# Performance work log

Measured on AMD Instinct MI355X. Metric: run time of the kernel, lower is better.

## Reference

```python
import jax, jax.numpy as jnp
import numpy as np

B, S, DM, H = 2, 2048, 1024, 16
HD = DM // H
SCALE = 1.0 / np.sqrt(HD)  # temperature = 1.0
LN_EPS = 1e-5


def setup_inputs() -> dict:
    key = jax.random.key(0)
    ks = jax.random.split(key, 12)
    s = 1.0 / np.sqrt(DM)
    inp = {
        'x': jax.random.normal(ks[0], (B, S, DM), dtype=jnp.float32),
        'Wq': jax.random.uniform(ks[1], (DM, DM), jnp.float32, -s, s),
        'bq': jnp.zeros((DM,), jnp.float32),
        'Wk': jax.random.uniform(ks[2], (DM, DM), jnp.float32, -s, s),
        'bk': jnp.zeros((DM,), jnp.float32),
        'Wv': jax.random.uniform(ks[3], (DM, DM), jnp.float32, -s, s),
        'bv': jnp.zeros((DM,), jnp.float32),
        'Wo': jax.random.uniform(ks[4], (DM, DM), jnp.float32, -s, s),
        'bo': jnp.zeros((DM,), jnp.float32),
        'Wg': jax.random.uniform(ks[5], (DM, DM), jnp.float32, -s, s),
        'bg': jnp.zeros((DM,), jnp.float32),
        'attention_weights': jnp.ones((H,), jnp.float32),
        'ln_gamma': jnp.ones((DM,), jnp.float32),
        'ln_beta': jnp.zeros((DM,), jnp.float32),
    }
    return inp


def _forward(x, Wq, bq, Wk, bk, Wv, bv, Wo, bo, Wg, bg, attention_weights, ln_gamma, ln_beta):
    # projections -> [B, H, S, HD]
    def split_heads(t):
        return t.reshape(B, S, H, HD).transpose(0, 2, 1, 3)
    q = split_heads(x @ Wq.T + bq)
    k = split_heads(x @ Wk.T + bk)
    v = split_heads(x @ Wv.T + bv)
    # scores [B, H, S, S]; no softmax: exact-erf GELU activation instead
    scores = jnp.einsum('bhsd,bhtd->bhst', q, k) * SCALE
    attn = jax.nn.gelu(scores, approximate=False)
    head_w = jax.nn.softmax(attention_weights)  # [H]
    attn = attn * head_w[None, :, None, None]
    # context [B, S, DM]
    ctx = jnp.einsum('bhst,bhtd->bhsd', attn, v).transpose(0, 2, 1, 3).reshape(B, S, DM)
    out = ctx @ Wo.T + bo
    gate = jax.nn.sigmoid(out @ Wg.T + bg)
    out = gate * out + (1.0 - gate) * x
    y = out + x
    mu = jnp.mean(y, axis=-1, keepdims=True)
    var = jnp.var(y, axis=-1, keepdims=True)
    return (y - mu) / jnp.sqrt(var + LN_EPS) * ln_gamma + ln_beta


def reference(x, Wq, bq, Wk, bk, Wv, bv, Wo, bo, Wg, bg, attention_weights, ln_gamma, ln_beta):
    return _forward(x, Wq, bq, Wk, bk, Wv, bv, Wo, bo, Wg, bg, attention_weights, ln_gamma, ln_beta)
```

## Files before the change

### kernel.cpp

```cpp
#include <hip/hip_runtime.h>
#include <hip/hip_bf16.h>

#define B_ 2
#define S_ 2048
#define DM_ 1024
#define H_ 16
#define HD_ 64
#define QKVLD 3072
#define WELT_ ((size_t)DM_ * DM_)

using bf16x8 = __attribute__((ext_vector_type(8))) short;
using f32x4  = __attribute__((ext_vector_type(4))) float;
using f32x16 = __attribute__((ext_vector_type(16))) float;

#define GLOAD16(g, l) __builtin_amdgcn_global_load_lds( \
    (const __attribute__((address_space(1))) void*)(g), \
    (__attribute__((address_space(3))) void*)(l), 16, 0, 0)

__device__ __forceinline__ int swz128(int row, int bytecol) {
    return row * 128 + (bytecol ^ ((row & 7) << 4));
}

__device__ __forceinline__ float gelu_poly(float x) {
    float u = x * x;
    float t = fmaf(-0.00074855f, u, 0.0146724f);
    t = fmaf(t, u, -0.1266945f);
    t = fmaf(t, u, 0.7966101f);
    float e = x * t;
    e = fminf(fmaxf(e, -1.0f), 1.0f);
    float hx = 0.5f * x;
    return fmaf(hx, e, hx);
}

__device__ __forceinline__ ushort bf16_rne(float f) {
    uint b = __builtin_bit_cast(uint, f);
    b += 0x7FFF + ((b >> 16) & 1);
    return (ushort)(b >> 16);
}

__device__ __forceinline__ float bf16_to_f(ushort u) {
    return __builtin_bit_cast(float, (uint)u << 16);
}

__device__ __forceinline__ uint cvtpk(float lo, float hi) {
    uint r;
    asm("v_cvt_pk_bf16_f32 %0, %1, %2" : "=v"(r) : "v"(lo), "v"(hi));
    return r;
}
__device__ __forceinline__ void pl32swap(uint& a, uint& b) {
    asm volatile("v_permlane32_swap_b32 %0, %1" : "+v"(a), "+v"(b));
}

__global__ __launch_bounds__(256) void cast_bf16_kernel(const float* __restrict__ in,
                                                        __hip_bfloat16* __restrict__ out, int n) {
    int i = (blockIdx.x * 256 + threadIdx.x) * 4;
    if (i >= n) return;
    float4 v = *(const float4*)(in + i);
    ushort4 o = { bf16_rne(v.x), bf16_rne(v.y), bf16_rne(v.z), bf16_rne(v.w) };
    *(ushort4*)(out + i) = o;
}

__global__ __launch_bounds__(256) void prep_kernel(
    const float* __restrict__ Wq, const float* __restrict__ Wk, const float* __restrict__ Wv,
    const float* __restrict__ Wo, const float* __restrict__ Wg,
    const float* __restrict__ bq, const float* __restrict__ bk, const float* __restrict__ bv,
    const float* __restrict__ aw, __hip_bfloat16* __restrict__ Wdst, float* __restrict__ bqkv)
{
    auto headw = [&](int h) {
        float mx = aw[0];
        for (int i = 1; i < H_; ++i) mx = fmaxf(mx, aw[i]);
        float sm = 0.f;
        for (int i = 0; i < H_; ++i) sm += expf(aw[i] - mx);
        return expf(aw[h] - mx) / sm;
    };
    int blk = blockIdx.x;
    if (blk < 5120) {
        int widx = blk >> 10;
        int row = blk & 1023;
        int off = row * 1024 + threadIdx.x * 4;
        const float* src = widx == 0 ? Wq : widx == 1 ? Wk : widx == 2 ? Wv : widx == 3 ? Wo : Wg;
        float scale = widx == 0 ? 0.125f : 1.0f;
        if (widx == 2) scale = headw(row >> 6);
        float4 v = *(const float4*)(src + off);
        ushort4 o = { bf16_rne(v.x * scale), bf16_rne(v.y * scale),
                      bf16_rne(v.z * scale), bf16_rne(v.w * scale) };
        *(ushort4*)(Wdst + widx * WELT_ + off) = o;
    } else {
        int i = (blk - 5120) * 256 + threadIdx.x;
        if (i < 3 * DM_) {
            float v;
            if (i < DM_) v = bq[i] * 0.125f;
            else if (i < 2 * DM_) v = bk[i - DM_];
            else v = bv[i - 2 * DM_] * headw((i - 2 * DM_) >> 6);
            bqkv[i] = v;
        }
    }
}

__global__ __launch_bounds__(256, 2) void gemm_nt_kernel(
    const __hip_bfloat16* __restrict__ A, int lda,
    const __hip_bfloat16* __restrict__ Bw, int ldb,
    const float* __restrict__ bias, float* __restrict__ Cf,
    __hip_bfloat16* __restrict__ Cb, int ldc, int M, int N, int K)
{
    __shared__ __align__(16) char smem[32768];
    const int tid = threadIdx.x;
    const int w = tid >> 6, lane = tid & 63, hi = lane >> 4, lo = lane & 15;
    const int wr = w >> 1, wc = w & 1;
    const int m0 = blockIdx.y * 128, n0 = blockIdx.x * 128;

    const int srow = lane >> 3;
    const int scol = (lane & 7) ^ srow;
    const __hip_bfloat16* sbase;
    int sld;
    char* lbase;
    if (w < 2) {
        sbase = A + (size_t)(m0 + w * 64 + srow) * lda + scol * 8;
        sld = lda;
        lbase = smem + w * 8192;
    } else {
        sbase = Bw + (size_t)(n0 + (w - 2) * 64 + srow) * ldb + scol * 8;
        sld = ldb;
        lbase = smem + 16384 + (w - 2) * 8192;
    }

    f32x4 acc[4][4];
#pragma unroll
    for (int m = 0; m < 4; ++m)
#pragma unroll
        for (int n = 0; n < 4; ++n) acc[m][n] = (f32x4){0.f, 0.f, 0.f, 0.f};

    for (int k0 = 0; k0 < K; k0 += 64) {
#pragma unroll
        for (int i = 0; i < 8; ++i)
            GLOAD16(sbase + (size_t)i * 8 * sld + k0, lbase + i * 1024);
        __syncthreads();
#pragma unroll
        for (int ks = 0; ks < 2; ++ks) {
            bf16x8 af[4], bfr[4];
#pragma unroll
            for (int m = 0; m < 4; ++m)
                af[m] = *(const bf16x8*)(smem + swz128(wr * 64 + m * 16 + lo, ks * 64 + hi * 16));
#pragma unroll
            for (int n = 0; n < 4; ++n)
                bfr[n] = *(const bf16x8*)(smem + 16384 + swz128(wc * 64 + n * 16 + lo, ks * 64 + hi * 16));
#pragma unroll
            for (int m = 0; m < 4; ++m)
#pragma unroll
                for (int n = 0; n < 4; ++n)
                    acc[m][n] = __builtin_amdgcn_mfma_f32_16x16x32_bf16(af[m], bfr[n], acc[m][n], 0, 0, 0);
        }
        __syncthreads();
    }

#pragma unroll
    for (int n = 0; n < 4; ++n) {
        int gc = n0 + wc * 64 + n * 16 + lo;
        float bz = bias[gc];
#pragma unroll
        for (int m = 0; m < 4; ++m) {
            int gr = m0 + wr * 64 + m * 16 + hi * 4;
#pragma unroll
            for (int r = 0; r < 4; ++r) {
                float v = acc[m][n][r] + bz;
                size_t o = (size_t)(gr + r) * ldc + gc;
                if (Cf) Cf[o] = v;
                if (Cb) *(ushort*)(Cb + o) = bf16_rne(v);
            }
        }
    }
}

__global__ __launch_bounds__(256) void transpose_v_kernel(const __hip_bfloat16* __restrict__ QKV,
                                                          __hip_bfloat16* __restrict__ Vt) {
    __shared__ __align__(16) ushort tile[64][80];
    const int tid = threadIdx.x;
    const int nt = S_ / 64;
    const int blk = blockIdx.x;
    const int t0 = (blk % nt) * 64;
    const int bh = blk / nt;
    const int h = bh % H_, b = bh / H_;
#pragma unroll
    for (int c = tid; c < 512; c += 256) {
        int row = c >> 3, cg = c & 7;
        float4 v = *(const float4*)(QKV + (size_t)(b * S_ + t0 + row) * QKVLD + 2 * DM_ + h * HD_ + cg * 8);
        *(float4*)(&tile[row][cg * 8]) = v;
    }
    __syncthreads();
#pragma unroll
    for (int c = tid; c < 512; c += 256) {
        int d = c >> 3, tg = c & 7;
        union { ushort u[8]; float4 v; } tmp;
#pragma unroll
        for (int j = 0; j < 8; ++j) tmp.u[j] = tile[tg * 8 + j][d];
        *(float4*)(Vt + ((size_t)(b * H_ + h) * HD_ + d) * S_ + t0 + tg * 8) = tmp.v;
    }
}

__global__ __launch_bounds__(256) void attn_kernel(
    const __hip_bfloat16* __restrict__ QKV, const __hip_bfloat16* __restrict__ Vt,
    __hip_bfloat16* __restrict__ ctx)
{
    __shared__ __align__(16) char lds[2][16384];

    const int tid = threadIdx.x;
    const int w = tid >> 6, lane = tid & 63;
    const int l31 = lane & 31, hi2 = lane >> 5;
    const int nq = S_ / 128;
    int blk = blockIdx.x;
    blk = (blk & 7) * 64 + (blk >> 3);
    const int q0 = (blk % nq) * 128;
    const int bh = blk / nq;
    const int h = bh % H_, b = bh / H_;

    bf16x8 qf[4];
    {
        const __hip_bfloat16* qrow = QKV + ((size_t)(b * S_ + q0 + w * 32 + l31) * QKVLD + h * HD_);
#pragma unroll
        for (int ks = 0; ks < 4; ++ks)
            qf[ks] = *(const bf16x8*)(qrow + ks * 16 + hi2 * 8);
    }

    const bool isK = (w < 2);
    const int fb = (w & 1) * 4;
    const __hip_bfloat16* sp[4];
    int ldsoff[4];
#pragma unroll
    for (int j = 0; j < 4; ++j) {
        int f = fb + j;
        if (isK) {
            sp[j] = QKV + (size_t)(b * S_ + (f >> 2) * 32 + l31) * QKVLD + DM_ + h * HD_ + (f & 3) * 16 + hi2 * 8;
            ldsoff[j] = f * 1024;
        } else {
            sp[j] = Vt + ((size_t)((b * H_ + h) * HD_) + (f >> 2) * 32 + l31) * S_ + (f & 3) * 16 + hi2 * 8;
            ldsoff[j] = 8192 + f * 1024;
        }
    }
    const size_t tstep = isK ? (size_t)64 * QKVLD : (size_t)64;

#define STAGE(buf) do { \
    _Pragma("unroll") \
    for (int j = 0; j < 4; ++j) { \
        GLOAD16(sp[j], lds[buf] + ldsoff[j]); \
        sp[j] += tstep; \
    } } while (0)

    f32x16 cacc[2];
#pragma unroll
    for (int n = 0; n < 2; ++n)
#pragma unroll
        for (int r = 0; r < 16; ++r) cacc[n][r] = 0.f;

    STAGE(0);
    asm volatile("s_waitcnt vmcnt(0)" ::: "memory");
    __builtin_amdgcn_s_barrier();

    const int lane16 = lane * 16;
    for (int t = 0; t < S_ / 64; ++t) {
        const int cur = t & 1;
        if (t + 1 < S_ / 64) STAGE(cur ^ 1);

#pragma unroll
        for (int n = 0; n < 2; ++n) {
            f32x16 sacc;
#pragma unroll
            for (int r = 0; r < 16; ++r) sacc[r] = 0.f;
#pragma unroll
            for (int ks = 0; ks < 4; ++ks) {
                bf16x8 kf = *(const bf16x8*)(lds[cur] + (n * 4 + ks) * 1024 + lane16);
                sacc = __builtin_amdgcn_mfma_f32_32x32x16_bf16(kf, qf[ks], sacc, 0, 0, 0);
            }
            float p[16];
#pragma unroll
            for (int r = 0; r < 16; ++r) p[r] = gelu_poly(sacc[r]);
            uint a0 = cvtpk(p[0], p[1]),   b0 = cvtpk(p[4], p[5]);
            uint a1 = cvtpk(p[2], p[3]),   b1 = cvtpk(p[6], p[7]);
            uint a2 = cvtpk(p[8], p[9]),   b2 = cvtpk(p[12], p[13]);
            uint a3 = cvtpk(p[10], p[11]), b3 = cvtpk(p[14], p[15]);
            pl32swap(a0, b0); pl32swap(a1, b1); pl32swap(a2, b2); pl32swap(a3, b3);
            union { uint u[4]; bf16x8 v; } pa0, pa1;
            pa0.u[0] = a0; pa0.u[1] = a1; pa0.u[2] = b0; pa0.u[3] = b1;
            pa1.u[0] = a2; pa1.u[1] = a3; pa1.u[2] = b2; pa1.u[3] = b3;
#pragma unroll
            for (int kc2 = 0; kc2 < 2; ++kc2) {
                int kc = n * 2 + kc2;
                bf16x8 pa = kc2 ? pa1.v : pa0.v;
#pragma unroll
                for (int n2 = 0; n2 < 2; ++n2) {
                    bf16x8 vf = *(const bf16x8*)(lds[cur] + 8192 + (n2 * 4 + kc) * 1024 + lane16);
                    cacc[n2] = __builtin_amdgcn_mfma_f32_32x32x16_bf16(pa, vf, cacc[n2], 0, 0, 0);
                }
            }
        }
        asm volatile("s_waitcnt vmcnt(0)" ::: "memory");
        __builtin_amdgcn_s_barrier();
    }

#pragma unroll
    for (int n2 = 0; n2 < 2; ++n2)
#pragma unroll
        for (int r = 0; r < 16; ++r) {
            int qrow = (r & 3) + 8 * (r >> 2) + 4 * hi2;
            size_t o = (size_t)(b * S_ + q0 + w * 32 + qrow) * DM_ + h * HD_ + n2 * 32 + l31;
            *(ushort*)(ctx + o) = bf16_rne(cacc[n2][r]);
        }
#undef STAGE
}

__global__ __launch_bounds__(256) void epilogue_ln_kernel(
    const __hip_bfloat16* __restrict__ outb, const __hip_bfloat16* __restrict__ gpreb,
    const float* __restrict__ x, const float* __restrict__ gamma,
    const float* __restrict__ beta, float* __restrict__ y)
{
    const int row = blockIdx.x, tid = threadIdx.x;
    const size_t base = (size_t)row * DM_ + tid * 4;
    ushort4 ob = *(const ushort4*)(outb + base);
    ushort4 gb = *(const ushort4*)(gpreb + base);
    float4 xv = *(const float4*)(x + base);
    float yv[4];
    float s = 0.f, s2 = 0.f;
    const ushort* obp = (const ushort*)&ob;
    const ushort* gbp = (const ushort*)&gb;
#pragma unroll
    for (int j = 0; j < 4; ++j) {
        float o = bf16_to_f(obp[j]), g = bf16_to_f(gbp[j]), xx = ((float*)&xv)[j];
        float gate = __builtin_amdgcn_rcpf(1.f + __expf(-g));
        float yy = gate * o + (1.f - gate) * xx + xx;
        yv[j] = yy;
        s += yy; s2 += yy * yy;
    }
    const int w = tid >> 6, lane = tid & 63;
#pragma unroll
    for (int off = 32; off > 0; off >>= 1) {
        s  += __shfl_down(s, off, 64);
        s2 += __shfl_down(s2, off, 64);
    }
    __shared__ float red[8];
    if (lane == 0) { red[w] = s; red[4 + w] = s2; }
    __syncthreads();
    s  = red[0] + red[1] + red[2] + red[3];
    s2 = red[4] + red[5] + red[6] + red[7];
    const float mu = s * (1.f / DM_);
    const float var = s2 * (1.f / DM_) - mu * mu;
    const float rstd = rsqrtf(var + 1e-5f);
    float4 outv;
#pragma unroll
    for (int j = 0; j < 4; ++j) {
        int col = tid * 4 + j;
        ((float*)&outv)[j] = (yv[j] - mu) * rstd * gamma[col] + beta[col];
    }
    *(float4*)(y + base) = outv;
}

extern "C" void kernel_launch(void* const* d_in, const int* in_sizes, int n_in,
                              void* d_out, int out_size, void* d_ws, size_t ws_size,
                              hipStream_t stream) {
    const float* x  = (const float*)d_in[0];
    const float* Wq = (const float*)d_in[1];
    const float* bq = (const float*)d_in[2];
    const float* Wk = (const float*)d_in[3];
    const float* bk = (const float*)d_in[4];
    const float* Wv = (const float*)d_in[5];
    const float* bv = (const float*)d_in[6];
    const float* Wo = (const float*)d_in[7];
    const float* bo = (const float*)d_in[8];
    const float* Wg = (const float*)d_in[9];
    const float* bg = (const float*)d_in[10];
    const float* aw = (const float*)d_in[11];
    const float* gamma = (const float*)d_in[12];
    const float* beta  = (const float*)d_in[13];

    char* ws = (char*)d_ws;
    size_t off = 0;
    auto alloc = [&](size_t bytes) -> char* {
        char* p = ws + off;
        off += (bytes + 255) & ~(size_t)255;
        return p;
    };
    const size_t NTOK = (size_t)B_ * S_;
    const size_t NELT = NTOK * DM_;

    __hip_bfloat16* xb    = (__hip_bfloat16*)alloc(NELT * 2);
    __hip_bfloat16* Wall  = (__hip_bfloat16*)alloc(5 * WELT_ * 2);
    float*          bqkv  = (float*)alloc(3 * DM_ * 4);
    __hip_bfloat16* qkvb  = (__hip_bfloat16*)alloc(NTOK * QKVLD * 2);
    __hip_bfloat16* Vtb   = (__hip_bfloat16*)alloc(NELT * 2);
    __hip_bfloat16* ctxb  = (__hip_bfloat16*)alloc(NELT * 2);
    __hip_bfloat16* outb  = (__hip_bfloat16*)alloc(NELT * 2);
    __hip_bfloat16* gpreb = (__hip_bfloat16*)alloc(NELT * 2);

    cast_bf16_kernel<<<(int)(NELT / 1024), 256, 0, stream>>>(x, xb, (int)NELT);
    prep_kernel<<<5120 + 12, 256, 0, stream>>>(Wq, Wk, Wv, Wo, Wg, bq, bk, bv, aw, Wall, bqkv);

    gemm_nt_kernel<<<dim3(QKVLD / 128, (int)(NTOK / 128)), 256, 0, stream>>>(
        xb, DM_, Wall, DM_, bqkv, nullptr, qkvb, QKVLD, (int)NTOK, QKVLD, DM_);

    transpose_v_kernel<<<B_ * H_ * (S_ / 64), 256, 0, stream>>>(qkvb, Vtb);
    attn_kernel<<<B_ * H_ * (S_ / 128), 256, 0, stream>>>(qkvb, Vtb, ctxb);

    gemm_nt_kernel<<<dim3(DM_ / 128, (int)(NTOK / 128)), 256, 0, stream>>>(
        ctxb, DM_, Wall + 3 * WELT_, DM_, bo, nullptr, outb, DM_, (int)NTOK, DM_, DM_);
    gemm_nt_kernel<<<dim3(DM_ / 128, (int)(NTOK / 128)), 256, 0, stream>>>(
        outb, DM_, Wall + 4 * WELT_, DM_, bg, nullptr, gpreb, DM_, (int)NTOK, DM_, DM_);

    epilogue_ln_kernel<<<(int)NTOK, 256, 0, stream>>>(outb, gpreb, x, gamma, beta, (float*)d_out);
}
```

Before: 162.1 us.

## Fold Wo into gate weights, triple-buffer attention, pack GELU math

Precomputes a combined weight Wg·Wo (via a small 1024^3 GEMM on transposed Wo) and a combined bias, so the output and gate projections become one N=2048 GEMM on ctx instead of two dependent GEMMs. The x cast is merged into the prep kernel to save a launch. The attention loop moves from double to triple buffering with a partial vmcnt wait, and the GELU polynomial uses packed f32 mul/fma instructions. Folding the weights changes the rounding path (gate input now comes from a bf16 product matrix), and the extra LDS buffer may lower attention occupancy.

Result: slower. 172.2 us (+6.3%).

```diff
diff --git a/kernel.cpp b/kernel.cpp
--- a/kernel.cpp
+++ b/kernel.cpp
@@ -10,6 +10,7 @@
 #define WELT_ ((size_t)DM_ * DM_)
 
 using bf16x8 = __attribute__((ext_vector_type(8))) short;
+using f32x2  = __attribute__((ext_vector_type(2))) float;
 using f32x4  = __attribute__((ext_vector_type(4))) float;
 using f32x16 = __attribute__((ext_vector_type(16))) float;
 
@@ -19,17 +20,6 @@
 
 __device__ __forceinline__ int swz128(int row, int bytecol) {
     return row * 128 + (bytecol ^ ((row & 7) << 4));
-}
-
-__device__ __forceinline__ float gelu_poly(float x) {
-    float u = x * x;
-    float t = fmaf(-0.00074855f, u, 0.0146724f);
-    t = fmaf(t, u, -0.1266945f);
-    t = fmaf(t, u, 0.7966101f);
-    float e = x * t;
-    e = fminf(fmaxf(e, -1.0f), 1.0f);
-    float hx = 0.5f * x;
-    return fmaf(hx, e, hx);
 }
 
 __device__ __forceinline__ ushort bf16_rne(float f) {
@@ -50,21 +40,24 @@
 __device__ __forceinline__ void pl32swap(uint& a, uint& b) {
     asm volatile("v_permlane32_swap_b32 %0, %1" : "+v"(a), "+v"(b));
 }
-
-__global__ __launch_bounds__(256) void cast_bf16_kernel(const float* __restrict__ in,
-                                                        __hip_bfloat16* __restrict__ out, int n) {
-    int i = (blockIdx.x * 256 + threadIdx.x) * 4;
-    if (i >= n) return;
-    float4 v = *(const float4*)(in + i);
-    ushort4 o = { bf16_rne(v.x), bf16_rne(v.y), bf16_rne(v.z), bf16_rne(v.w) };
-    *(ushort4*)(out + i) = o;
+__device__ __forceinline__ f32x2 pk_mul(f32x2 a, f32x2 b) {
+    f32x2 d;
+    asm("v_pk_mul_f32 %0, %1, %2" : "=v"(d) : "v"(a), "v"(b));
+    return d;
+}
+__device__ __forceinline__ f32x2 pk_fma(f32x2 a, f32x2 b, f32x2 c) {
+    f32x2 d;
+    asm("v_pk_fma_f32 %0, %1, %2, %3" : "=v"(d) : "v"(a), "v"(b), "v"(c));
+    return d;
 }
 
 __global__ __launch_bounds__(256) void prep_kernel(
+    const float* __restrict__ x, __hip_bfloat16* __restrict__ xb,
     const float* __restrict__ Wq, const float* __restrict__ Wk, const float* __restrict__ Wv,
     const float* __restrict__ Wo, const float* __restrict__ Wg,
     const float* __restrict__ bq, const float* __restrict__ bk, const float* __restrict__ bv,
-    const float* __restrict__ aw, __hip_bfloat16* __restrict__ Wdst, float* __restrict__ bqkv)
+    const float* __restrict__ aw, __hip_bfloat16* __restrict__ Wall,
+    __hip_bfloat16* __restrict__ Wcomb, float* __restrict__ bqkv)
 {
     auto headw = [&](int h) {
         float mx = aw[0];
@@ -74,19 +67,27 @@
         return expf(aw[h] - mx) / sm;
     };
     int blk = blockIdx.x;
-    if (blk < 5120) {
+    if (blk < 4096) {
+        int i = blk * 1024 + threadIdx.x * 4;
+        float4 v = *(const float4*)(x + i);
+        ushort4 o = { bf16_rne(v.x), bf16_rne(v.y), bf16_rne(v.z), bf16_rne(v.w) };
+        *(ushort4*)(xb + i) = o;
+    } else if (blk < 9216) {
+        blk -= 4096;
         int widx = blk >> 10;
         int row = blk & 1023;
         int off = row * 1024 + threadIdx.x * 4;
         const float* src = widx == 0 ? Wq : widx == 1 ? Wk : widx == 2 ? Wv : widx == 3 ? Wo : Wg;
         float scale = widx == 0 ? 0.125f : 1.0f;
         if (widx == 2) scale = headw(row >> 6);
+        __hip_bfloat16* dst = (widx == 3) ? Wcomb
+                            : Wall + (size_t)(widx == 4 ? 3 : widx) * WELT_;
         float4 v = *(const float4*)(src + off);
         ushort4 o = { bf16_rne(v.x * scale), bf16_rne(v.y * scale),
                       bf16_rne(v.z * scale), bf16_rne(v.w * scale) };
-        *(ushort4*)(Wdst + widx * WELT_ + off) = o;
+        *(ushort4*)(dst + off) = o;
     } else {
-        int i = (blk - 5120) * 256 + threadIdx.x;
+        int i = (blk - 9216) * 256 + threadIdx.x;
         if (i < 3 * DM_) {
             float v;
             if (i < DM_) v = bq[i] * 0.125f;
@@ -95,6 +96,45 @@
             bqkv[i] = v;
         }
     }
+}
+
+__global__ __launch_bounds__(256) void transpose_wo_kernel(const float* __restrict__ Wo,
+                                                           __hip_bfloat16* __restrict__ Wot) {
+    __shared__ ushort tile[64][72];
+    const int tid = threadIdx.x;
+    const int c0 = blockIdx.x * 64, r0 = blockIdx.y * 64;
+#pragma unroll
+    for (int c = tid; c < 1024; c += 256) {
+        int row = c >> 4, cg = c & 15;
+        float4 v = *(const float4*)(Wo + (size_t)(r0 + row) * 1024 + c0 + cg * 4);
+        tile[row][cg * 4 + 0] = bf16_rne(v.x);
+        tile[row][cg * 4 + 1] = bf16_rne(v.y);
+        tile[row][cg * 4 + 2] = bf16_rne(v.z);
+        tile[row][cg * 4 + 3] = bf16_rne(v.w);
+    }
+    __syncthreads();
+#pragma unroll
+    for (int c = tid; c < 512; c += 256) {
+        int d = c >> 3, tg = c & 7;
+        union { ushort u[8]; float4 v; } tmp;
+#pragma unroll
+        for (int j = 0; j < 8; ++j) tmp.u[j] = tile[tg * 8 + j][d];
+        *(float4*)(Wot + (size_t)(c0 + d) * 1024 + r0 + tg * 8) = tmp.v;
+    }
+}
+
+__global__ __launch_bounds__(256) void bias2_kernel(const float* __restrict__ Wg,
+                                                    const float* __restrict__ bo,
+                                                    const float* __restrict__ bg,
+                                                    float* __restrict__ bcomb) {
+    const int tid = threadIdx.x, w = tid >> 6, lane = tid & 63;
+    if (blockIdx.x < 4) bcomb[blockIdx.x * 256 + tid] = bo[blockIdx.x * 256 + tid];
+    const int row = blockIdx.x * 4 + w;
+    float s = 0.f;
+    for (int k = lane; k < 1024; k += 64) s += Wg[row * 1024 + k] * bo[k];
+#pragma unroll
+    for (int off = 32; off > 0; off >>= 1) s += __shfl_down(s, off, 64);
+    if (lane == 0) bcomb[1024 + row] = bg[row] + s;
 }
 
 __global__ __launch_bounds__(256, 2) void gemm_nt_kernel(
@@ -156,7 +196,7 @@
 #pragma unroll
     for (int n = 0; n < 4; ++n) {
         int gc = n0 + wc * 64 + n * 16 + lo;
-        float bz = bias[gc];
+        float bz = bias ? bias[gc] : 0.f;
 #pragma unroll
         for (int m = 0; m < 4; ++m) {
             int gr = m0 + wr * 64 + m * 16 + hi * 4;
@@ -201,7 +241,7 @@
     const __hip_bfloat16* __restrict__ QKV, const __hip_bfloat16* __restrict__ Vt,
     __hip_bfloat16* __restrict__ ctx)
 {
-    __shared__ __align__(16) char lds[2][16384];
+    __shared__ __align__(16) char lds[3 * 16384];
 
     const int tid = threadIdx.x;
     const int w = tid >> 6, lane = tid & 63;
@@ -238,28 +278,28 @@
     }
     const size_t tstep = isK ? (size_t)64 * QKVLD : (size_t)64;
 
-#define STAGE(buf) do { \
+#define STAGE(base) do { \
     _Pragma("unroll") \
     for (int j = 0; j < 4; ++j) { \
-        GLOAD16(sp[j], lds[buf] + ldsoff[j]); \
+        GLOAD16(sp[j], (base) + ldsoff[j]); \
         sp[j] += tstep; \
     } } while (0)
 
+    const f32x2 PC3 = {-0.00074855f, -0.00074855f};
+    const f32x2 PC2 = { 0.0146724f,   0.0146724f};
+    const f32x2 PC1 = {-0.1266945f,  -0.1266945f};
+    const f32x2 PC0 = { 0.7966101f,   0.7966101f};
+    const f32x2 PHALF = {0.5f, 0.5f};
+
     f32x16 cacc[2];
 #pragma unroll
     for (int n = 0; n < 2; ++n)
 #pragma unroll
         for (int r = 0; r < 16; ++r) cacc[n][r] = 0.f;
 
-    STAGE(0);
-    asm volatile("s_waitcnt vmcnt(0)" ::: "memory");
-    __builtin_amdgcn_s_barrier();
-
     const int lane16 = lane * 16;
-    for (int t = 0; t < S_ / 64; ++t) {
-        const int cur = t & 1;
-        if (t + 1 < S_ / 64) STAGE(cur ^ 1);
-
+
+    auto compute_tile = [&](const char* cbase) {
 #pragma unroll
         for (int n = 0; n < 2; ++n) {
             f32x16 sacc;
@@ -267,16 +307,27 @@
             for (int r = 0; r < 16; ++r) sacc[r] = 0.f;
 #pragma unroll
             for (int ks = 0; ks < 4; ++ks) {
-                bf16x8 kf = *(const bf16x8*)(lds[cur] + (n * 4 + ks) * 1024 + lane16);
+                bf16x8 kf = *(const bf16x8*)(cbase + (n * 4 + ks) * 1024 + lane16);
                 sacc = __builtin_amdgcn_mfma_f32_32x32x16_bf16(kf, qf[ks], sacc, 0, 0, 0);
             }
-            float p[16];
-#pragma unroll
-            for (int r = 0; r < 16; ++r) p[r] = gelu_poly(sacc[r]);
-            uint a0 = cvtpk(p[0], p[1]),   b0 = cvtpk(p[4], p[5]);
-            uint a1 = cvtpk(p[2], p[3]),   b1 = cvtpk(p[6], p[7]);
-            uint a2 = cvtpk(p[8], p[9]),   b2 = cvtpk(p[12], p[13]);
-            uint a3 = cvtpk(p[10], p[11]), b3 = cvtpk(p[14], p[15]);
+            f32x2 P[8];
+#pragma unroll
+            for (int i = 0; i < 8; ++i) {
+                f32x2 xv = { sacc[2 * i], sacc[2 * i + 1] };
+                f32x2 u  = pk_mul(xv, xv);
+                f32x2 tt = pk_fma(PC3, u, PC2);
+                tt = pk_fma(tt, u, PC1);
+                tt = pk_fma(tt, u, PC0);
+                f32x2 e  = pk_mul(xv, tt);
+                e[0] = fminf(fmaxf(e[0], -1.f), 1.f);
+                e[1] = fminf(fmaxf(e[1], -1.f), 1.f);
+                f32x2 hx = pk_mul(xv, PHALF);
+                P[i] = pk_fma(hx, e, hx);
+            }
+            uint a0 = cvtpk(P[0][0], P[0][1]), b0 = cvtpk(P[2][0], P[2][1]);
+            uint a1 = cvtpk(P[1][0], P[1][1]), b1 = cvtpk(P[3][0], P[3][1]);
+            uint a2 = cvtpk(P[4][0], P[4][1]), b2 = cvtpk(P[6][0], P[6][1]);
+            uint a3 = cvtpk(P[5][0], P[5][1]), b3 = cvtpk(P[7][0], P[7][1]);
             pl32swap(a0, b0); pl32swap(a1, b1); pl32swap(a2, b2); pl32swap(a3, b3);
             union { uint u[4]; bf16x8 v; } pa0, pa1;
             pa0.u[0] = a0; pa0.u[1] = a1; pa0.u[2] = b0; pa0.u[3] = b1;
@@ -287,14 +338,31 @@
                 bf16x8 pa = kc2 ? pa1.v : pa0.v;
 #pragma unroll
                 for (int n2 = 0; n2 < 2; ++n2) {
-                    bf16x8 vf = *(const bf16x8*)(lds[cur] + 8192 + (n2 * 4 + kc) * 1024 + lane16);
+                    bf16x8 vf = *(const bf16x8*)(cbase + 8192 + (n2 * 4 + kc) * 1024 + lane16);
                     cacc[n2] = __builtin_amdgcn_mfma_f32_32x32x16_bf16(pa, vf, cacc[n2], 0, 0, 0);
                 }
             }
         }
-        asm volatile("s_waitcnt vmcnt(0)" ::: "memory");
+    };
+
+    const int NT = S_ / 64;
+    STAGE(lds);
+    STAGE(lds + 16384);
+
+    int cur = 0;
+    for (int t = 0; t < NT - 1; ++t) {
+        asm volatile("s_waitcnt vmcnt(4)" ::: "memory");
         __builtin_amdgcn_s_barrier();
-    }
+        if (t + 2 < NT) {
+            int nb = cur + 2; if (nb >= 3) nb -= 3;
+            STAGE(lds + nb * 16384);
+        }
+        compute_tile(lds + cur * 16384);
+        cur = (cur == 2) ? 0 : cur + 1;
+    }
+    asm volatile("s_waitcnt vmcnt(0)" ::: "memory");
+    __builtin_amdgcn_s_barrier();
+    compute_tile(lds + cur * 16384);
 
 #pragma unroll
     for (int n2 = 0; n2 < 2; ++n2)
@@ -308,15 +376,16 @@
 }
 
 __global__ __launch_bounds__(256) void epilogue_ln_kernel(
-    const __hip_bfloat16* __restrict__ outb, const __hip_bfloat16* __restrict__ gpreb,
-    const float* __restrict__ x, const float* __restrict__ gamma,
-    const float* __restrict__ beta, float* __restrict__ y)
+    const __hip_bfloat16* __restrict__ og, const float* __restrict__ x,
+    const float* __restrict__ gamma, const float* __restrict__ beta,
+    float* __restrict__ y)
 {
     const int row = blockIdx.x, tid = threadIdx.x;
-    const size_t base = (size_t)row * DM_ + tid * 4;
-    ushort4 ob = *(const ushort4*)(outb + base);
-    ushort4 gb = *(const ushort4*)(gpreb + base);
-    float4 xv = *(const float4*)(x + base);
+    const size_t obase = (size_t)row * 2048 + tid * 4;
+    const size_t xbase = (size_t)row * DM_ + tid * 4;
+    ushort4 ob = *(const ushort4*)(og + obase);
+    ushort4 gb = *(const ushort4*)(og + obase + 1024);
+    float4 xv = *(const float4*)(x + xbase);
     float yv[4];
     float s = 0.f, s2 = 0.f;
     const ushort* obp = (const ushort*)&ob;
@@ -349,7 +418,7 @@
         int col = tid * 4 + j;
         ((float*)&outv)[j] = (yv[j] - mu) * rstd * gamma[col] + beta[col];
     }
-    *(float4*)(y + base) = outv;
+    *(float4*)(y + xbase) = outv;
 }
 
 extern "C" void kernel_launch(void* const* d_in, const int* in_sizes, int n_in,
@@ -381,16 +450,24 @@
     const size_t NELT = NTOK * DM_;
 
     __hip_bfloat16* xb    = (__hip_bfloat16*)alloc(NELT * 2);
-    __hip_bfloat16* Wall  = (__hip_bfloat16*)alloc(5 * WELT_ * 2);
+    __hip_bfloat16* Wall  = (__hip_bfloat16*)alloc(4 * WELT_ * 2);
+    __hip_bfloat16* Wot   = (__hip_bfloat16*)alloc(WELT_ * 2);
+    __hip_bfloat16* Wcomb = (__hip_bfloat16*)alloc(2 * WELT_ * 2);
     float*          bqkv  = (float*)alloc(3 * DM_ * 4);
+    float*          bcomb = (float*)alloc(2 * DM_ * 4);
     __hip_bfloat16* qkvb  = (__hip_bfloat16*)alloc(NTOK * QKVLD * 2);
     __hip_bfloat16* Vtb   = (__hip_bfloat16*)alloc(NELT * 2);
     __hip_bfloat16* ctxb  = (__hip_bfloat16*)alloc(NELT * 2);
-    __hip_bfloat16* outb  = (__hip_bfloat16*)alloc(NELT * 2);
-    __hip_bfloat16* gpreb = (__hip_bfloat16*)alloc(NELT * 2);
-
-    cast_bf16_kernel<<<(int)(NELT / 1024), 256, 0, stream>>>(x, xb, (int)NELT);
-    prep_kernel<<<5120 + 12, 256, 0, stream>>>(Wq, Wk, Wv, Wo, Wg, bq, bk, bv, aw, Wall, bqkv);
+    __hip_bfloat16* ogb   = (__hip_bfloat16*)alloc(NTOK * 2048 * 2);
+
+    prep_kernel<<<9216 + 12, 256, 0, stream>>>(x, xb, Wq, Wk, Wv, Wo, Wg,
+                                               bq, bk, bv, aw, Wall, Wcomb, bqkv);
+    transpose_wo_kernel<<<dim3(16, 16), 256, 0, stream>>>(Wo, Wot);
+    bias2_kernel<<<256, 256, 0, stream>>>(Wg, bo, bg, bcomb);
+
+    gemm_nt_kernel<<<dim3(8, 8), 256, 0, stream>>>(
+        Wall + 3 * WELT_, DM_, Wot, DM_, nullptr, nullptr,
+        Wcomb + WELT_, DM_, DM_, DM_, DM_);
 
     gemm_nt_kernel<<<dim3(QKVLD / 128, (int)(NTOK / 128)), 256, 0, stream>>>(
         xb, DM_, Wall, DM_, bqkv, nullptr, qkvb, QKVLD, (int)NTOK, QKVLD, DM_);
@@ -398,10 +475,8 @@
     transpose_v_kernel<<<B_ * H_ * (S_ / 64), 256, 0, stream>>>(qkvb, Vtb);
     attn_kernel<<<B_ * H_ * (S_ / 128), 256, 0, stream>>>(qkvb, Vtb, ctxb);
 
-    gemm_nt_kernel<<<dim3(DM_ / 128, (int)(NTOK / 128)), 256, 0, stream>>>(
-        ctxb, DM_, Wall + 3 * WELT_, DM_, bo, nullptr, outb, DM_, (int)NTOK, DM_, DM_);
-    gemm_nt_kernel<<<dim3(DM_ / 128, (int)(NTOK / 128)), 256, 0, stream>>>(
-        outb, DM_, Wall + 4 * WELT_, DM_, bg, nullptr, gpreb, DM_, (int)NTOK, DM_, DM_);
-
-    epilogue_ln_kernel<<<(int)NTOK, 256, 0, stream>>>(outb, gpreb, x, gamma, beta, (float*)d_out);
-}
+    gemm_nt_kernel<<<dim3(2048 / 128, (int)(NTOK / 128)), 256, 0, stream>>>(
+        ctxb, DM_, Wcomb, DM_, bcomb, nullptr, ogb, 2048, (int)NTOK, 2048, DM_);
+
+    epilogue_ln_kernel<<<(int)NTOK, 256, 0, stream>>>(ogb, x, gamma, beta, (float*)d_out);
+}
```

## Fold gate projection into output GEMM and enlarge attention key tiles

Applied to the files above, without the earlier changes.

Precomputes Wg·Wo and bg+Wg·bo so that one N=2048 GEMM yields both the output and the gate pre-activation. This removes the dependent second 1024-wide GEMM and its intermediate buffer, at the cost of extra GEMM blocks that build the combined weight. The x cast is merged into the prep kernel, which also transposes Wo. The attention loop now stages 128-key tiles with double buffering and raises wave priority around the MFMA work. The epilogue reads the bf16 copy of x for the residual, which trades some accuracy for less memory traffic, and GELU clamping uses fmed3.

New measurement: 149.6 us. -7.7%, faster.

```diff
diff --git a/kernel.cpp b/kernel.cpp
--- a/kernel.cpp
+++ b/kernel.cpp
@@ -26,8 +26,7 @@
     float t = fmaf(-0.00074855f, u, 0.0146724f);
     t = fmaf(t, u, -0.1266945f);
     t = fmaf(t, u, 0.7966101f);
-    float e = x * t;
-    e = fminf(fmaxf(e, -1.0f), 1.0f);
+    float e = __builtin_amdgcn_fmed3f(x * t, -1.0f, 1.0f);
     float hx = 0.5f * x;
     return fmaf(hx, e, hx);
 }
@@ -51,21 +50,17 @@
     asm volatile("v_permlane32_swap_b32 %0, %1" : "+v"(a), "+v"(b));
 }
 
-__global__ __launch_bounds__(256) void cast_bf16_kernel(const float* __restrict__ in,
-                                                        __hip_bfloat16* __restrict__ out, int n) {
-    int i = (blockIdx.x * 256 + threadIdx.x) * 4;
-    if (i >= n) return;
-    float4 v = *(const float4*)(in + i);
-    ushort4 o = { bf16_rne(v.x), bf16_rne(v.y), bf16_rne(v.z), bf16_rne(v.w) };
-    *(ushort4*)(out + i) = o;
-}
-
 __global__ __launch_bounds__(256) void prep_kernel(
+    const float* __restrict__ x, __hip_bfloat16* __restrict__ xb,
     const float* __restrict__ Wq, const float* __restrict__ Wk, const float* __restrict__ Wv,
     const float* __restrict__ Wo, const float* __restrict__ Wg,
     const float* __restrict__ bq, const float* __restrict__ bk, const float* __restrict__ bv,
-    const float* __restrict__ aw, __hip_bfloat16* __restrict__ Wdst, float* __restrict__ bqkv)
+    const float* __restrict__ bo, const float* __restrict__ bg,
+    const float* __restrict__ aw, __hip_bfloat16* __restrict__ Wall,
+    __hip_bfloat16* __restrict__ Wcomb, __hip_bfloat16* __restrict__ Wot,
+    float* __restrict__ bqkv, float* __restrict__ bcomb)
 {
+    __shared__ ushort stile[64][72];
     auto headw = [&](int h) {
         float mx = aw[0];
         for (int i = 1; i < H_; ++i) mx = fmaxf(mx, aw[i]);
@@ -73,20 +68,29 @@
         for (int i = 0; i < H_; ++i) sm += expf(aw[i] - mx);
         return expf(aw[h] - mx) / sm;
     };
+    const int tid = threadIdx.x;
     int blk = blockIdx.x;
-    if (blk < 5120) {
+    if (blk < 4096) {
+        int i = blk * 1024 + tid * 4;
+        float4 v = *(const float4*)(x + i);
+        ushort4 o = { bf16_rne(v.x), bf16_rne(v.y), bf16_rne(v.z), bf16_rne(v.w) };
+        *(ushort4*)(xb + i) = o;
+    } else if (blk < 9216) {
+        blk -= 4096;
         int widx = blk >> 10;
         int row = blk & 1023;
-        int off = row * 1024 + threadIdx.x * 4;
+        int off = row * 1024 + tid * 4;
         const float* src = widx == 0 ? Wq : widx == 1 ? Wk : widx == 2 ? Wv : widx == 3 ? Wo : Wg;
         float scale = widx == 0 ? 0.125f : 1.0f;
         if (widx == 2) scale = headw(row >> 6);
+        __hip_bfloat16* dst = (widx == 3) ? Wcomb
+                            : Wall + (size_t)(widx == 4 ? 3 : widx) * WELT_;
         float4 v = *(const float4*)(src + off);
         ushort4 o = { bf16_rne(v.x * scale), bf16_rne(v.y * scale),
                       bf16_rne(v.z * scale), bf16_rne(v.w * scale) };
-        *(ushort4*)(Wdst + widx * WELT_ + off) = o;
-    } else {
-        int i = (blk - 5120) * 256 + threadIdx.x;
+        *(ushort4*)(dst + off) = o;
+    } else if (blk < 9228) {
+        int i = (blk - 9216) * 256 + tid;
         if (i < 3 * DM_) {
             float v;
             if (i < DM_) v = bq[i] * 0.125f;
@@ -94,6 +98,37 @@
             else v = bv[i - 2 * DM_] * headw((i - 2 * DM_) >> 6);
             bqkv[i] = v;
         }
+    } else if (blk < 9484) {
+        int idx = blk - 9228;
+        const int c0 = (idx & 15) * 64, r0 = (idx >> 4) * 64;
+#pragma unroll
+        for (int c = tid; c < 1024; c += 256) {
+            int row = c >> 4, cg = c & 15;
+            float4 v = *(const float4*)(Wo + (size_t)(r0 + row) * 1024 + c0 + cg * 4);
+            stile[row][cg * 4 + 0] = bf16_rne(v.x);
+            stile[row][cg * 4 + 1] = bf16_rne(v.y);
+            stile[row][cg * 4 + 2] = bf16_rne(v.z);
+            stile[row][cg * 4 + 3] = bf16_rne(v.w);
+        }
+        __syncthreads();
+#pragma unroll
+        for (int c = tid; c < 512; c += 256) {
+            int d = c >> 3, tg = c & 7;
+            union { ushort u[8]; float4 v; } tmp;
+#pragma unroll
+            for (int j = 0; j < 8; ++j) tmp.u[j] = stile[tg * 8 + j][d];
+            *(float4*)(Wot + (size_t)(c0 + d) * 1024 + r0 + tg * 8) = tmp.v;
+        }
+    } else {
+        int idx = blk - 9484;
+        const int w = tid >> 6, lane = tid & 63;
+        if (idx < 4) bcomb[idx * 256 + tid] = bo[idx * 256 + tid];
+        const int row = idx * 4 + w;
+        float s = 0.f;
+        for (int k = lane; k < 1024; k += 64) s += Wg[row * 1024 + k] * bo[k];
+#pragma unroll
+        for (int off = 32; off > 0; off >>= 1) s += __shfl_down(s, off, 64);
+        if (lane == 0) bcomb[1024 + row] = bg[row] + s;
     }
 }
 
@@ -101,13 +136,32 @@
     const __hip_bfloat16* __restrict__ A, int lda,
     const __hip_bfloat16* __restrict__ Bw, int ldb,
     const float* __restrict__ bias, float* __restrict__ Cf,
-    __hip_bfloat16* __restrict__ Cb, int ldc, int M, int N, int K)
+    __hip_bfloat16* __restrict__ Cb, int ldc, int K, int gx1, int nblk1,
+    const __hip_bfloat16* __restrict__ A2, const __hip_bfloat16* __restrict__ B2,
+    __hip_bfloat16* __restrict__ C2)
 {
     __shared__ __align__(16) char smem[32768];
     const int tid = threadIdx.x;
     const int w = tid >> 6, lane = tid & 63, hi = lane >> 4, lo = lane & 15;
     const int wr = w >> 1, wc = w & 1;
-    const int m0 = blockIdx.y * 128, n0 = blockIdx.x * 128;
+
+    const int bid = blockIdx.x;
+    const __hip_bfloat16 *Ap, *Bp;
+    const float* bp;
+    float* cf;
+    __hip_bfloat16* cb;
+    int LDA, LDB, LDC, KK, bx, by;
+    if (bid < nblk1) {
+        bx = bid % gx1; by = bid / gx1;
+        Ap = A; Bp = Bw; bp = bias; cf = Cf; cb = Cb;
+        LDA = lda; LDB = ldb; LDC = ldc; KK = K;
+    } else {
+        int t2 = bid - nblk1;
+        bx = t2 & 7; by = t2 >> 3;
+        Ap = A2; Bp = B2; bp = nullptr; cf = nullptr; cb = C2;
+        LDA = DM_; LDB = DM_; LDC = DM_; KK = DM_;
+    }
+    const int m0 = by * 128, n0 = bx * 128;
 
     const int srow = lane >> 3;
     const int scol = (lane & 7) ^ srow;
@@ -115,12 +169,12 @@
     int sld;
     char* lbase;
     if (w < 2) {
-        sbase = A + (size_t)(m0 + w * 64 + srow) * lda + scol * 8;
-        sld = lda;
+        sbase = Ap + (size_t)(m0 + w * 64 + srow) * LDA + scol * 8;
+        sld = LDA;
         lbase = smem + w * 8192;
     } else {
-        sbase = Bw + (size_t)(n0 + (w - 2) * 64 + srow) * ldb + scol * 8;
-        sld = ldb;
+        sbase = Bp + (size_t)(n0 + (w - 2) * 64 + srow) * LDB + scol * 8;
+        sld = LDB;
         lbase = smem + 16384 + (w - 2) * 8192;
     }
 
@@ -130,7 +184,7 @@
 #pragma unroll
         for (int n = 0; n < 4; ++n) acc[m][n] = (f32x4){0.f, 0.f, 0.f, 0.f};
 
-    for (int k0 = 0; k0 < K; k0 += 64) {
+    for (int k0 = 0; k0 < KK; k0 += 64) {
 #pragma unroll
         for (int i = 0; i < 8; ++i)
             GLOAD16(sbase + (size_t)i * 8 * sld + k0, lbase + i * 1024);
@@ -156,16 +210,16 @@
 #pragma unroll
     for (int n = 0; n < 4; ++n) {
         int gc = n0 + wc * 64 + n * 16 + lo;
-        float bz = bias[gc];
+        float bz = bp ? bp[gc] : 0.f;
 #pragma unroll
         for (int m = 0; m < 4; ++m) {
             int gr = m0 + wr * 64 + m * 16 + hi * 4;
 #pragma unroll
             for (int r = 0; r < 4; ++r) {
                 float v = acc[m][n][r] + bz;
-                size_t o = (size_t)(gr + r) * ldc + gc;
-                if (Cf) Cf[o] = v;
-                if (Cb) *(ushort*)(Cb + o) = bf16_rne(v);
+                size_t o = (size_t)(gr + r) * LDC + gc;
+                if (cf) cf[o] = v;
+                if (cb) *(ushort*)(cb + o) = bf16_rne(v);
             }
         }
     }
@@ -201,7 +255,7 @@
     const __hip_bfloat16* __restrict__ QKV, const __hip_bfloat16* __restrict__ Vt,
     __hip_bfloat16* __restrict__ ctx)
 {
-    __shared__ __align__(16) char lds[2][16384];
+    __shared__ __align__(16) char lds[2][32768];
 
     const int tid = threadIdx.x;
     const int w = tid >> 6, lane = tid & 63;
@@ -222,26 +276,26 @@
     }
 
     const bool isK = (w < 2);
-    const int fb = (w & 1) * 4;
-    const __hip_bfloat16* sp[4];
-    int ldsoff[4];
-#pragma unroll
-    for (int j = 0; j < 4; ++j) {
-        int f = fb + j;
+    const int f0 = (w & 1) * 8;
+    const __hip_bfloat16* sp[8];
+    int loff[8];
+#pragma unroll
+    for (int j = 0; j < 8; ++j) {
+        int f = f0 + j;
         if (isK) {
             sp[j] = QKV + (size_t)(b * S_ + (f >> 2) * 32 + l31) * QKVLD + DM_ + h * HD_ + (f & 3) * 16 + hi2 * 8;
-            ldsoff[j] = f * 1024;
+            loff[j] = f * 1024;
         } else {
-            sp[j] = Vt + ((size_t)((b * H_ + h) * HD_) + (f >> 2) * 32 + l31) * S_ + (f & 3) * 16 + hi2 * 8;
-            ldsoff[j] = 8192 + f * 1024;
-        }
-    }
-    const size_t tstep = isK ? (size_t)64 * QKVLD : (size_t)64;
+            sp[j] = Vt + ((size_t)((b * H_ + h) * HD_) + (f >> 3) * 32 + l31) * S_ + (f & 7) * 16 + hi2 * 8;
+            loff[j] = 16384 + f * 1024;
+        }
+    }
+    const size_t tstep = isK ? (size_t)128 * QKVLD : (size_t)128;
 
 #define STAGE(buf) do { \
     _Pragma("unroll") \
-    for (int j = 0; j < 4; ++j) { \
-        GLOAD16(sp[j], lds[buf] + ldsoff[j]); \
+    for (int j = 0; j < 8; ++j) { \
+        GLOAD16(sp[j], lds[buf] + loff[j]); \
         sp[j] += tstep; \
     } } while (0)
 
@@ -256,18 +310,20 @@
     __builtin_amdgcn_s_barrier();
 
     const int lane16 = lane * 16;
-    for (int t = 0; t < S_ / 64; ++t) {
+    const int NT = S_ / 128;
+    for (int t = 0; t < NT; ++t) {
         const int cur = t & 1;
-        if (t + 1 < S_ / 64) STAGE(cur ^ 1);
-
-#pragma unroll
-        for (int n = 0; n < 2; ++n) {
+        if (t + 1 < NT) STAGE(cur ^ 1);
+
+        __builtin_amdgcn_s_setprio(1);
+#pragma unroll
+        for (int tc = 0; tc < 4; ++tc) {
             f32x16 sacc;
 #pragma unroll
             for (int r = 0; r < 16; ++r) sacc[r] = 0.f;
 #pragma unroll
             for (int ks = 0; ks < 4; ++ks) {
-                bf16x8 kf = *(const bf16x8*)(lds[cur] + (n * 4 + ks) * 1024 + lane16);
+                bf16x8 kf = *(const bf16x8*)(lds[cur] + (tc * 4 + ks) * 1024 + lane16);
                 sacc = __builtin_amdgcn_mfma_f32_32x32x16_bf16(kf, qf[ks], sacc, 0, 0, 0);
             }
             float p[16];
@@ -283,15 +339,16 @@
             pa1.u[0] = a2; pa1.u[1] = a3; pa1.u[2] = b2; pa1.u[3] = b3;
 #pragma unroll
             for (int kc2 = 0; kc2 < 2; ++kc2) {
-                int kc = n * 2 + kc2;
+                int kc = tc * 2 + kc2;
                 bf16x8 pa = kc2 ? pa1.v : pa0.v;
 #pragma unroll
                 for (int n2 = 0; n2 < 2; ++n2) {
-                    bf16x8 vf = *(const bf16x8*)(lds[cur] + 8192 + (n2 * 4 + kc) * 1024 + lane16);
+                    bf16x8 vf = *(const bf16x8*)(lds[cur] + 16384 + (n2 * 8 + kc) * 1024 + lane16);
                     cacc[n2] = __builtin_amdgcn_mfma_f32_32x32x16_bf16(pa, vf, cacc[n2], 0, 0, 0);
                 }
             }
         }
+        __builtin_amdgcn_s_setprio(0);
         asm volatile("s_waitcnt vmcnt(0)" ::: "memory");
         __builtin_amdgcn_s_barrier();
     }
@@ -308,22 +365,24 @@
 }
 
 __global__ __launch_bounds__(256) void epilogue_ln_kernel(
-    const __hip_bfloat16* __restrict__ outb, const __hip_bfloat16* __restrict__ gpreb,
-    const float* __restrict__ x, const float* __restrict__ gamma,
-    const float* __restrict__ beta, float* __restrict__ y)
+    const __hip_bfloat16* __restrict__ og, const __hip_bfloat16* __restrict__ xb,
+    const float* __restrict__ gamma, const float* __restrict__ beta,
+    float* __restrict__ y)
 {
     const int row = blockIdx.x, tid = threadIdx.x;
-    const size_t base = (size_t)row * DM_ + tid * 4;
-    ushort4 ob = *(const ushort4*)(outb + base);
-    ushort4 gb = *(const ushort4*)(gpreb + base);
-    float4 xv = *(const float4*)(x + base);
+    const size_t obase = (size_t)row * 2048 + tid * 4;
+    const size_t xbase = (size_t)row * DM_ + tid * 4;
+    ushort4 ob = *(const ushort4*)(og + obase);
+    ushort4 gb = *(const ushort4*)(og + obase + 1024);
+    ushort4 xv = *(const ushort4*)(xb + xbase);
     float yv[4];
     float s = 0.f, s2 = 0.f;
     const ushort* obp = (const ushort*)&ob;
     const ushort* gbp = (const ushort*)&gb;
+    const ushort* xp  = (const ushort*)&xv;
 #pragma unroll
     for (int j = 0; j < 4; ++j) {
-        float o = bf16_to_f(obp[j]), g = bf16_to_f(gbp[j]), xx = ((float*)&xv)[j];
+        float o = bf16_to_f(obp[j]), g = bf16_to_f(gbp[j]), xx = bf16_to_f(xp[j]);
         float gate = __builtin_amdgcn_rcpf(1.f + __expf(-g));
         float yy = gate * o + (1.f - gate) * xx + xx;
         yv[j] = yy;
@@ -349,7 +408,7 @@
         int col = tid * 4 + j;
         ((float*)&outv)[j] = (yv[j] - mu) * rstd * gamma[col] + beta[col];
     }
-    *(float4*)(y + base) = outv;
+    *(float4*)(y + xbase) = outv;
 }
 
 extern "C" void kernel_launch(void* const* d_in, const int* in_sizes, int n_in,
@@ -381,27 +440,30 @@
     const size_t NELT = NTOK * DM_;
 
     __hip_bfloat16* xb    = (__hip_bfloat16*)alloc(NELT * 2);
-    __hip_bfloat16* Wall  = (__hip_bfloat16*)alloc(5 * WELT_ * 2);
+    __hip_bfloat16* Wall  = (__hip_bfloat16*)alloc(4 * WELT_ * 2);
+    __hip_bfloat16* Wot   = (__hip_bfloat16*)alloc(WELT_ * 2);
+    __hip_bfloat16* Wcomb = (__hip_bfloat16*)alloc(2 * WELT_ * 2);
     float*          bqkv  = (float*)alloc(3 * DM_ * 4);
+    float*          bcomb = (float*)alloc(2 * DM_ * 4);
     __hip_bfloat16* qkvb  = (__hip_bfloat16*)alloc(NTOK * QKVLD * 2);
     __hip_bfloat16* Vtb   = (__hip_bfloat16*)alloc(NELT * 2);
     __hip_bfloat16* ctxb  = (__hip_bfloat16*)alloc(NELT * 2);
-    __hip_bfloat16* outb  = (__hip_bfloat16*)alloc(NELT * 2);
-    __hip_bfloat16* gpreb = (__hip_bfloat16*)alloc(NELT * 2);
-
-    cast_bf16_kernel<<<(int)(NELT / 1024), 256, 0, stream>>>(x, xb, (int)NELT);
-    prep_kernel<<<5120 + 12, 256, 0, stream>>>(Wq, Wk, Wv, Wo, Wg, bq, bk, bv, aw, Wall, bqkv);
-
-    gemm_nt_kernel<<<dim3(QKVLD / 128, (int)(NTOK / 128)), 256, 0, stream>>>(
-        xb, DM_, Wall, DM_, bqkv, nullptr, qkvb, QKVLD, (int)NTOK, QKVLD, DM_);
+    __hip_bfloat16* ogb   = (__hip_bfloat16*)alloc(NTOK * 2048 * 2);
+
+    prep_kernel<<<9740, 256, 0, stream>>>(x, xb, Wq, Wk, Wv, Wo, Wg,
+                                          bq, bk, bv, bo, bg, aw,
+                                          Wall, Wcomb, Wot, bqkv, bcomb);
+
+    gemm_nt_kernel<<<768 + 64, 256, 0, stream>>>(
+        xb, DM_, Wall, DM_, bqkv, nullptr, qkvb, QKVLD, DM_, 24, 768,
+        Wall + 3 * WELT_, Wot, Wcomb + WELT_);
 
     transpose_v_kernel<<<B_ * H_ * (S_ / 64), 256, 0, stream>>>(qkvb, Vtb);
     attn_kernel<<<B_ * H_ * (S_ / 128), 256, 0, stream>>>(qkvb, Vtb, ctxb);
 
-    gemm_nt_kernel<<<dim3(DM_ / 128, (int)(NTOK / 128)), 256, 0, stream>>>(
-        ctxb, DM_, Wall + 3 * WELT_, DM_, bo, nullptr, outb, DM_, (int)NTOK, DM_, DM_);
-    gemm_nt_kernel<<<dim3(DM_ / 128, (int)(NTOK / 128)), 256, 0, stream>>>(
-        outb, DM_, Wall + 4 * WELT_, DM_, bg, nullptr, gpreb, DM_, (int)NTOK, DM_, DM_);
-
-    epilogue_ln_kernel<<<(int)NTOK, 256, 0, stream>>>(outb, gpreb, x, gamma, beta, (float*)d_out);
-}
+    gemm_nt_kernel<<<512, 256, 0, stream>>>(
+        ctxb, DM_, Wcomb, DM_, bcomb, nullptr, ogb, 2048, DM_, 16, 1 << 30,
+        nullptr, nullptr, nullptr);
+
+    epilogue_ln_kernel<<<(int)NTOK, 256, 0, stream>>>(ogb, xb, gamma, beta, (float*)d_out);
+}
```
